# Performance work log

Hardware: AMD Instinct MI355X
Metric: run time of the kernel (lower is better)

## Reference

```python
import jax, jax.numpy as jnp
import numpy as np

E = 768       # embedding_dim
H = 12        # num_heads
ID = 768      # inter_dim
HD = ID // H  # head_dim = 64
DHX = HD // 2  # 32
DHY = HD - DHX  # 32
HP, WP = 16, 16
P = HP * WP
BASE = 10000.0
SCALE = HD ** -0.5


def rot_half(x):
    x1 = x[..., 0::2]
    x2 = x[..., 1::2]
    return jnp.stack([-x2, x1], axis=-1).reshape(x.shape)


def apply_rope(x, cos, sin):
    cos = jnp.repeat(cos, 2, axis=-1)
    sin = jnp.repeat(sin, 2, axis=-1)
    return x * cos + rot_half(x) * sin


def rope_cache(L, dim, base):
    inv_freq = 1.0 / base ** (jnp.arange(0, dim, 2, dtype=jnp.float32) / dim)
    t = jnp.arange(L, dtype=jnp.float32)
    freqs = t[:, None] * inv_freq[None, :]  # [L, dim//2]
    return jnp.cos(freqs), jnp.sin(freqs)


def _rope_tables():
    yy, xx = jnp.meshgrid(jnp.arange(HP), jnp.arange(WP), indexing='ij')
    py = yy.reshape(P)
    px = xx.reshape(P)
    cos_x, sin_x = rope_cache(WP, DHX, BASE)
    cos_y, sin_y = rope_cache(HP, DHY, BASE)
    # gather per-patch tables, shape (1,1,P,1,D/2)
    cx = cos_x[px].reshape(1, 1, P, 1, DHX // 2)
    sx = sin_x[px].reshape(1, 1, P, 1, DHX // 2)
    cy = cos_y[py].reshape(1, 1, P, 1, DHY // 2)
    sy = sin_y[py].reshape(1, 1, P, 1, DHY // 2)
    return cx, sx, cy, sy


def setup_inputs() -> dict:
    key = jax.random.key(0)
    ks = jax.random.split(key, 8)
    B, T = 8, 16
    x = jax.random.normal(ks[0], (B, T, P, E), dtype=jnp.float32)
    s = 0.02
    return {
        'x': x,
        'Wq': jax.random.normal(ks[1], (E, ID), dtype=jnp.float32) * s,
        'bq': jnp.zeros((ID,), dtype=jnp.float32),
        'Wk': jax.random.normal(ks[2], (E, ID), dtype=jnp.float32) * s,
        'bk': jnp.zeros((ID,), dtype=jnp.float32),
        'Wv': jax.random.normal(ks[3], (E, ID), dtype=jnp.float32) * s,
        'bv': jnp.zeros((ID,), dtype=jnp.float32),
        'Wo': jax.random.normal(ks[4], (ID, E), dtype=jnp.float32) * s,
    }


def reference(x, Wq, bq, Wk, bk, Wv, bv, Wo):
    B, T, Pn, _ = x.shape
    q = (x @ Wq + bq).reshape(B, T, Pn, H, HD)
    k = (x @ Wk + bk).reshape(B, T, Pn, H, HD)
    v = (x @ Wv + bv).reshape(B, T, Pn, H, HD)

    cx, sx, cy, sy = _rope_tables()
    qx, qy = q[..., :DHX], q[..., DHX:]
    kx, ky = k[..., :DHX], k[..., DHX:]
    q = jnp.concatenate([apply_rope(qx, cx, sx), apply_rope(qy, cy, sy)], axis=-1)
    k = jnp.concatenate([apply_rope(kx, cx, sx), apply_rope(ky, cy, sy)], axis=-1)

    scores = jnp.einsum('btihd,btjhd->bthij', q, k) * SCALE
    probs = jax.nn.softmax(scores, axis=-1)
    y = jnp.einsum('bthij,btjhd->btihd', probs, v).reshape(B, T, Pn, ID)
    return y @ Wo
```

## Files before the change

kernel.cpp:

```cpp
#include <hip/hip_runtime.h>
#include <hip/hip_bf16.h>
#include <cstdint>
#include <cstddef>

typedef __bf16 bf16;
typedef __bf16 bf16x8 __attribute__((ext_vector_type(8)));
typedef __bf16 bf16x4 __attribute__((ext_vector_type(4)));
typedef float  f32x4  __attribute__((ext_vector_type(4)));

#define MFMA_BF16(a,b,c) __builtin_amdgcn_mfma_f32_16x16x32_bf16((a),(b),(c),0,0,0)

#define BB 8
#define TT 16
#define PP 256
#define EE 768
#define HH 12
#define HDD 64
#define NQKV 2304
#define MROWS 32768

__device__ __forceinline__ void gld_lds16(const bf16* g, bf16* l) {
  __builtin_amdgcn_global_load_lds((const __attribute__((address_space(1))) void*)g,
                                   (__attribute__((address_space(3))) void*)l, 16, 0, 0);
}

__global__ __launch_bounds__(256) void k_cvt_x(const float* __restrict__ x,
                                               bf16* __restrict__ xb) {
  const int64_t i = (int64_t)blockIdx.x * 256 + threadIdx.x;
  const float4* src = (const float4*)x;
  float4 a = src[i * 2];
  float4 b = src[i * 2 + 1];
  bf16x8 o;
  o[0] = (bf16)a.x; o[1] = (bf16)a.y; o[2] = (bf16)a.z; o[3] = (bf16)a.w;
  o[4] = (bf16)b.x; o[5] = (bf16)b.y; o[6] = (bf16)b.z; o[7] = (bf16)b.w;
  *(bf16x8*)(xb + i * 8) = o;
}

__global__ __launch_bounds__(256) void k_wt(const float* __restrict__ Wq,
                                            const float* __restrict__ Wk,
                                            const float* __restrict__ Wv,
                                            const float* __restrict__ Wo,
                                            bf16* __restrict__ wt) {
  __shared__ float tile[32][33];
  const int n0 = blockIdx.x * 32;
  const int k0 = blockIdx.y * 32;
  const float* W;
  int nc;
  if (n0 < 768)        { W = Wq; nc = n0; }
  else if (n0 < 1536)  { W = Wk; nc = n0 - 768; }
  else if (n0 < 2304)  { W = Wv; nc = n0 - 1536; }
  else                 { W = Wo; nc = n0 - 2304; }
  const int tx = threadIdx.x & 31, ty = threadIdx.x >> 5;
  for (int r = ty; r < 32; r += 8)
    tile[r][tx] = W[(int64_t)(k0 + r) * 768 + nc + tx];
  __syncthreads();
  for (int r = ty; r < 32; r += 8)
    wt[(int64_t)(n0 + r) * 768 + k0 + tx] = (bf16)tile[tx][r];
}

__global__ __launch_bounds__(512, 2) void k_qkv(const bf16* __restrict__ xb,
                                                const bf16* __restrict__ wt,
                                                const float* __restrict__ bq,
                                                const float* __restrict__ bk,
                                                const float* __restrict__ bv,
                                                bf16* __restrict__ qb,
                                                bf16* __restrict__ kb,
                                                bf16* __restrict__ vt) {
  extern __shared__ char smem_raw[];
  bf16* smem = (bf16*)smem_raw;
  const int tid = threadIdx.x;
  const int w = tid >> 6, lane = tid & 63, quad = lane >> 4, l16 = lane & 15;
  const int wr = w >> 2, wc = w & 3;
  const int bid = blockIdx.x;
  const int xcd = bid & 7;
  const int loc = bid >> 3;
  const int m0  = (xcd * 16 + loc / 9) * 256;
  const int n0  = (loc % 9) * 256;
  const int cg8 = (((lane & 3) ^ ((lane >> 3) & 3)) * 8);
  const bf16* Ag0 = xb + (int64_t)(m0 + w * 16 + (lane >> 2)) * 768 + cg8;
  const bf16* Bg0 = wt + (int64_t)(n0 + w * 16 + (lane >> 2)) * 768 + cg8;

  auto stage = [&](int kt, int b) {
    bf16* LA = smem + b * 16384 + w * 512;
    bf16* LB = LA + 8192;
    const bf16* GA = Ag0 + kt * 32;
    const bf16* GB = Bg0 + kt * 32;
    gld_lds16(GA, LA);
    gld_lds16(GA + 128 * 768, LA + 4096);
    gld_lds16(GB, LB);
    gld_lds16(GB + 128 * 768, LB + 4096);
  };

  f32x4 acc[8][4] = {};
  stage(0, 0);
  stage(1, 1);
  stage(2, 2);
  const int rkey8 = ((l16 >> 1) & 3) * 8;
  for (int t = 0; t < 24; ++t) {
    if (t < 22)       { asm volatile("s_waitcnt vmcnt(8)" ::: "memory"); }
    else if (t == 22) { asm volatile("s_waitcnt vmcnt(4)" ::: "memory"); }
    else              { asm volatile("s_waitcnt vmcnt(0)" ::: "memory"); }
    __builtin_amdgcn_s_barrier();
    __builtin_amdgcn_sched_barrier(0);
    if (t < 21) stage(t + 3, (t + 3) & 3);
    const bf16* A = smem + (t & 3) * 16384;
    const bf16* B = A + 8192;
    bf16x8 bfr[4];
#pragma unroll
    for (int ni = 0; ni < 4; ++ni)
      bfr[ni] = *(const bf16x8*)&B[(wc * 64 + ni * 16 + l16) * 32 + ((quad * 8) ^ rkey8)];
    bf16x8 afr[8];
#pragma unroll
    for (int mi = 0; mi < 8; ++mi)
      afr[mi] = *(const bf16x8*)&A[(wr * 128 + mi * 16 + l16) * 32 + ((quad * 8) ^ rkey8)];
    __builtin_amdgcn_s_setprio(1);
#pragma unroll
    for (int mi = 0; mi < 8; ++mi)
#pragma unroll
      for (int ni = 0; ni < 4; ++ni)
        acc[mi][ni] = MFMA_BF16(afr[mi], bfr[ni], acc[mi][ni]);
    __builtin_amdgcn_s_setprio(0);
  }
  const int sec = n0 / 768;
  const float* bias_p = (sec == 0) ? bq : (sec == 1) ? bk : bv;
  if (sec == 2) {
#pragma unroll
    for (int ni = 0; ni < 4; ++ni) {
      const int ng = (n0 % 768) + wc * 64 + ni * 16 + l16;
      const int h = ng >> 6, hd = ng & 63;
      const float bias = bias_p[ng];
#pragma unroll
      for (int mi = 0; mi < 8; ++mi) {
        const int rb = m0 + wr * 128 + mi * 16 + quad * 4;
        const int bt = rb >> 8, p = rb & 255;
        bf16x4 pk;
#pragma unroll
        for (int r = 0; r < 4; ++r) pk[r] = (bf16)(acc[mi][ni][r] + bias);
        *(bf16x4*)&vt[((int64_t)(bt * 12 + h) * 64 + hd) * 256 + p] = pk;
      }
    }
  } else {
    bf16* dst = (sec == 0) ? qb : kb;
    const float L2C = 0.83048202372184058696f;
#pragma unroll
    for (int ni = 0; ni < 4; ++ni) {
      const int ng = (n0 % 768) + wc * 64 + ni * 16 + l16;
      const int h = ng >> 6, hd = ng & 63;
      const float bias = bias_p[ng];
      const int j = (hd & 31) >> 1;
      const float invf = exp2f(-(float)j * L2C);
      const bool odd = (hd & 1);
      const bool isx = (hd < 32);
#pragma unroll
      for (int mi = 0; mi < 8; ++mi) {
        const int rb = m0 + wr * 128 + mi * 16 + quad * 4;
        const int bt = rb >> 8;
        const int pb = rb & 255;
#pragma unroll
        for (int r = 0; r < 4; ++r) {
          const int p = pb + r;
          float v = acc[mi][ni][r] + bias;
          float pv = __shfl_xor(v, 1, 64);
          const int pos = isx ? (p & 15) : (p >> 4);
          float sn, cs;
          __sincosf((float)pos * invf, &sn, &cs);
          float o = odd ? (v * cs + pv * sn) : (v * cs - pv * sn);
          dst[((int64_t)(bt * 12 + h) * 256 + p) * 64 + hd] = (bf16)o;
        }
      }
    }
  }
}

__global__ __launch_bounds__(256) void k_attn(bf16* qy,
                                              const bf16* __restrict__ kb,
                                              const bf16* __restrict__ vt) {
  __shared__ __align__(16) bf16 plds[4][16 * 264];
  const int tid = threadIdx.x;
  const int w = tid >> 6, lane = tid & 63, quad = lane >> 4, l16 = lane & 15;
  const int64_t base = (int64_t)blockIdx.x * 16384;
  bf16* Q = qy + base;
  const bf16* K = kb + base;
  const bf16* V = vt + base;
  bf16* pl = plds[w];
  for (int s = 0; s < 4; ++s) {
    const int r0 = w * 64 + s * 16;
    bf16x8 qf0 = *(const bf16x8*)&Q[(r0 + l16) * 64 + quad * 8];
    bf16x8 qf1 = *(const bf16x8*)&Q[(r0 + l16) * 64 + 32 + quad * 8];
    f32x4 sacc[16] = {};
#pragma unroll
    for (int ct = 0; ct < 16; ++ct) {
      bf16x8 kf0 = *(const bf16x8*)&K[(ct * 16 + l16) * 64 + quad * 8];
      bf16x8 kf1 = *(const bf16x8*)&K[(ct * 16 + l16) * 64 + 32 + quad * 8];
      sacc[ct] = MFMA_BF16(qf0, kf0, sacc[ct]);
      sacc[ct] = MFMA_BF16(qf1, kf1, sacc[ct]);
    }
    float mx[4] = {-3e38f, -3e38f, -3e38f, -3e38f};
#pragma unroll
    for (int ct = 0; ct < 16; ++ct)
#pragma unroll
      for (int r = 0; r < 4; ++r) mx[r] = fmaxf(mx[r], sacc[ct][r]);
#pragma unroll
    for (int d = 1; d < 16; d <<= 1)
#pragma unroll
      for (int r = 0; r < 4; ++r) mx[r] = fmaxf(mx[r], __shfl_xor(mx[r], d, 64));
    float sm[4] = {0.f, 0.f, 0.f, 0.f};
#pragma unroll
    for (int ct = 0; ct < 16; ++ct)
#pragma unroll
      for (int r = 0; r < 4; ++r) {
        float e = __expf((sacc[ct][r] - mx[r]) * 0.125f);
        sacc[ct][r] = e;
        sm[r] += e;
      }
#pragma unroll
    for (int d = 1; d < 16; d <<= 1)
#pragma unroll
      for (int r = 0; r < 4; ++r) sm[r] += __shfl_xor(sm[r], d, 64);
#pragma unroll
    for (int ct = 0; ct < 16; ++ct)
#pragma unroll
      for (int r = 0; r < 4; ++r)
        pl[(quad * 4 + r) * 264 + ct * 16 + l16] = (bf16)sacc[ct][r];
    __syncthreads();
    f32x4 oacc[4] = {};
#pragma unroll
    for (int kc = 0; kc < 8; ++kc) {
      bf16x8 pf = *(const bf16x8*)&pl[l16 * 264 + kc * 32 + quad * 8];
#pragma unroll
      for (int nt = 0; nt < 4; ++nt) {
        bf16x8 vf = *(const bf16x8*)&V[(nt * 16 + l16) * 256 + kc * 32 + quad * 8];
        oacc[nt] = MFMA_BF16(pf, vf, oacc[nt]);
      }
    }
    float inv[4];
#pragma unroll
    for (int r = 0; r < 4; ++r) inv[r] = 1.0f / sm[r];
#pragma unroll
    for (int nt = 0; nt < 4; ++nt)
#pragma unroll
      for (int r = 0; r < 4; ++r)
        Q[(r0 + quad * 4 + r) * 64 + nt * 16 + l16] = (bf16)(oacc[nt][r] * inv[r]);
    __syncthreads();
  }
}

__global__ __launch_bounds__(512, 2) void k_out(const bf16* __restrict__ yb,
                                                const bf16* __restrict__ wt,
                                                float* __restrict__ out) {
  extern __shared__ char smem_raw[];
  bf16* smem = (bf16*)smem_raw;
  const int tid = threadIdx.x;
  const int w = tid >> 6, lane = tid & 63, quad = lane >> 4, l16 = lane & 15;
  const int wr = w >> 1, wc = w & 1;
  const int bid = blockIdx.x;
  const int xcd = bid & 7;
  const int loc = bid >> 3;
  const int m0  = (xcd * 16 + loc / 6) * 256;
  const int n0  = (loc % 6) * 128;
  const int bt  = m0 >> 8;
  const int srow = w * 8 + (lane >> 3);
  const int cgo  = (((lane & 7) ^ ((lane >> 3) & 7)) * 8);
  const bf16* Bg0 = wt + (int64_t)(2304 + n0 + srow) * 768 + cgo;

  auto stage = [&](int kt, int p) {
    bf16* LA = smem + p * 24576 + w * 512;
    bf16* LB = smem + p * 24576 + 16384 + w * 512;
    const bf16* GA = yb + (int64_t)(bt * 12 + kt) * 16384 + srow * 64 + cgo;
    const bf16* GB = Bg0 + kt * 64;
#pragma unroll
    for (int rd = 0; rd < 4; ++rd)
      gld_lds16(GA + rd * 4096, LA + rd * 4096);
#pragma unroll
    for (int rd = 0; rd < 2; ++rd)
      gld_lds16(GB + rd * 49152, LB + rd * 4096);
  };

  f32x4 acc[4][4] = {};
  stage(0, 0);
  __syncthreads();
  const int rkey8 = (l16 & 7) * 8;
  for (int t = 0; t < 12; ++t) {
    if (t < 11) stage(t + 1, (t + 1) & 1);
    __builtin_amdgcn_sched_barrier(0);
    const bf16* A = smem + (t & 1) * 24576;
    const bf16* B = A + 16384;
    bf16x8 bfr[4][2];
#pragma unroll
    for (int ni = 0; ni < 4; ++ni)
#pragma unroll
      for (int kk = 0; kk < 2; ++kk)
        bfr[ni][kk] = *(const bf16x8*)&B[(wc * 64 + ni * 16 + l16) * 64 +
                                         (((kk * 4 + quad) * 8) ^ rkey8)];
    bf16x8 afr[4][2];
#pragma unroll
    for (int mi = 0; mi < 4; ++mi)
#pragma unroll
      for (int kk = 0; kk < 2; ++kk)
        afr[mi][kk] = *(const bf16x8*)&A[(wr * 64 + mi * 16 + l16) * 64 +
                                         (((kk * 4 + quad) * 8) ^ rkey8)];
    __builtin_amdgcn_s_setprio(1);
#pragma unroll
    for (int mi = 0; mi < 4; ++mi)
#pragma unroll
      for (int ni = 0; ni < 4; ++ni)
#pragma unroll
        for (int kk = 0; kk < 2; ++kk)
          acc[mi][ni] = MFMA_BF16(afr[mi][kk], bfr[ni][kk], acc[mi][ni]);
    __builtin_amdgcn_s_setprio(0);
    __syncthreads();
  }
#pragma unroll
  for (int mi = 0; mi < 4; ++mi)
#pragma unroll
    for (int ni = 0; ni < 4; ++ni) {
      const int rg = m0 + wr * 64 + mi * 16 + quad * 4;
      const int cg = n0 + wc * 64 + ni * 16 + l16;
#pragma unroll
      for (int r = 0; r < 4; ++r)
        out[(int64_t)(rg + r) * 768 + cg] = acc[mi][ni][r];
    }
}

extern "C" void kernel_launch(void* const* d_in, const int* in_sizes, int n_in,
                              void* d_out, int out_size, void* d_ws, size_t ws_size,
                              hipStream_t stream) {
  const float* x  = (const float*)d_in[0];
  const float* Wq = (const float*)d_in[1];
  const float* bq = (const float*)d_in[2];
  const float* Wk = (const float*)d_in[3];
  const float* bk = (const float*)d_in[4];
  const float* Wv = (const float*)d_in[5];
  const float* bv = (const float*)d_in[6];
  const float* Wo = (const float*)d_in[7];
  float* out = (float*)d_out;

  uint8_t* ws = (uint8_t*)d_ws;
  const size_t SZ = (size_t)25165824 * 2;
  bf16* qy = (bf16*)ws;
  bf16* kb = (bf16*)(ws + SZ);
  bf16* vt = (bf16*)(ws + 2 * SZ);
  bf16* wt = (bf16*)(ws + 3 * SZ);
  bf16* xb = (bf16*)d_out;

  static int attr_set = 0;
  if (!attr_set) {
    (void)hipFuncSetAttribute((const void*)k_qkv,
                              hipFuncAttributeMaxDynamicSharedMemorySize, 131072);
    (void)hipFuncSetAttribute((const void*)k_out,
                              hipFuncAttributeMaxDynamicSharedMemorySize, 98304);
    attr_set = 1;
  }

  k_cvt_x<<<12288, 256, 0, stream>>>(x, xb);
  k_wt<<<dim3(96, 24), 256, 0, stream>>>(Wq, Wk, Wv, Wo, wt);
  k_qkv<<<1152, 512, 131072, stream>>>(xb, wt, bq, bk, bv, qy, kb, vt);
  k_attn<<<1536, 256, 0, stream>>>(qy, kb, vt);
  k_out<<<768, 512, 98304, stream>>>(qy, wt, out);
}
```

Before: 537.0 us.

## Restage QKV GEMM with BK=64 double buffer and LDS-staged coalesced epilogue

```diff
diff --git a/kernel.cpp b/kernel.cpp
--- a/kernel.cpp
+++ b/kernel.cpp
@@ -71,103 +71,146 @@
   const int tid = threadIdx.x;
   const int w = tid >> 6, lane = tid & 63, quad = lane >> 4, l16 = lane & 15;
   const int wr = w >> 2, wc = w & 3;
+  const int kap = l16 & 7;
   const int bid = blockIdx.x;
   const int xcd = bid & 7;
   const int loc = bid >> 3;
   const int m0  = (xcd * 16 + loc / 9) * 256;
   const int n0  = (loc % 9) * 256;
-  const int cg8 = (((lane & 3) ^ ((lane >> 3) & 3)) * 8);
-  const bf16* Ag0 = xb + (int64_t)(m0 + w * 16 + (lane >> 2)) * 768 + cg8;
-  const bf16* Bg0 = wt + (int64_t)(n0 + w * 16 + (lane >> 2)) * 768 + cg8;
-
-  auto stage = [&](int kt, int b) {
-    bf16* LA = smem + b * 16384 + w * 512;
-    bf16* LB = LA + 8192;
-    const bf16* GA = Ag0 + kt * 32;
-    const bf16* GB = Bg0 + kt * 32;
-    gld_lds16(GA, LA);
-    gld_lds16(GA + 128 * 768, LA + 4096);
-    gld_lds16(GB, LB);
-    gld_lds16(GB + 128 * 768, LB + 4096);
+  const int srow = w * 8 + (lane >> 3);
+  const int cgo  = ((lane & 7) ^ ((lane >> 3) & 7)) * 8;
+  const bf16* Ag = xb + (int64_t)(m0 + srow) * 768 + cgo;
+  const bf16* Bg = wt + (int64_t)(n0 + srow) * 768 + cgo;
+
+  auto stage = [&](int kt, int p) {
+    bf16* LA = smem + p * 32768 + w * 512;
+    bf16* LB = LA + 16384;
+    const bf16* GA = Ag + kt * 64;
+    const bf16* GB = Bg + kt * 64;
+#pragma unroll
+    for (int rd = 0; rd < 4; ++rd) {
+      gld_lds16(GA + rd * 49152, LA + rd * 4096);
+      gld_lds16(GB + rd * 49152, LB + rd * 4096);
+    }
   };
 
   f32x4 acc[8][4] = {};
   stage(0, 0);
-  stage(1, 1);
-  stage(2, 2);
-  const int rkey8 = ((l16 >> 1) & 3) * 8;
-  for (int t = 0; t < 24; ++t) {
-    if (t < 22)       { asm volatile("s_waitcnt vmcnt(8)" ::: "memory"); }
-    else if (t == 22) { asm volatile("s_waitcnt vmcnt(4)" ::: "memory"); }
-    else              { asm volatile("s_waitcnt vmcnt(0)" ::: "memory"); }
-    __builtin_amdgcn_s_barrier();
+  __syncthreads();
+  for (int t = 0; t < 12; ++t) {
+    if (t < 11) stage(t + 1, (t + 1) & 1);
     __builtin_amdgcn_sched_barrier(0);
-    if (t < 21) stage(t + 3, (t + 3) & 3);
-    const bf16* A = smem + (t & 3) * 16384;
-    const bf16* B = A + 8192;
-    bf16x8 bfr[4];
+    const bf16* A = smem + (t & 1) * 32768;
+    const bf16* B = A + 16384;
+    bf16x8 bfr[4][2];
 #pragma unroll
     for (int ni = 0; ni < 4; ++ni)
-      bfr[ni] = *(const bf16x8*)&B[(wc * 64 + ni * 16 + l16) * 32 + ((quad * 8) ^ rkey8)];
-    bf16x8 afr[8];
-#pragma unroll
-    for (int mi = 0; mi < 8; ++mi)
-      afr[mi] = *(const bf16x8*)&A[(wr * 128 + mi * 16 + l16) * 32 + ((quad * 8) ^ rkey8)];
-    __builtin_amdgcn_s_setprio(1);
-#pragma unroll
-    for (int mi = 0; mi < 8; ++mi)
-#pragma unroll
-      for (int ni = 0; ni < 4; ++ni)
-        acc[mi][ni] = MFMA_BF16(afr[mi], bfr[ni], acc[mi][ni]);
-    __builtin_amdgcn_s_setprio(0);
+#pragma unroll
+      for (int kk = 0; kk < 2; ++kk)
+        bfr[ni][kk] = *(const bf16x8*)&B[(wc * 64 + ni * 16 + l16) * 64 +
+                                         (((kk * 4 + quad) ^ kap) * 8)];
+#pragma unroll
+    for (int mh = 0; mh < 2; ++mh) {
+      bf16x8 afr[4][2];
+#pragma unroll
+      for (int mi = 0; mi < 4; ++mi)
+#pragma unroll
+        for (int kk = 0; kk < 2; ++kk)
+          afr[mi][kk] = *(const bf16x8*)&A[(wr * 128 + mh * 64 + mi * 16 + l16) * 64 +
+                                           (((kk * 4 + quad) ^ kap) * 8)];
+      __builtin_amdgcn_s_setprio(1);
+#pragma unroll
+      for (int mi = 0; mi < 4; ++mi)
+#pragma unroll
+        for (int ni = 0; ni < 4; ++ni)
+#pragma unroll
+          for (int kk = 0; kk < 2; ++kk)
+            acc[mh * 4 + mi][ni] = MFMA_BF16(afr[mi][kk], bfr[ni][kk], acc[mh * 4 + mi][ni]);
+      __builtin_amdgcn_s_setprio(0);
+    }
+    __syncthreads();
   }
   const int sec = n0 / 768;
+  const int h0 = (n0 % 768) >> 6;
   const float* bias_p = (sec == 0) ? bq : (sec == 1) ? bk : bv;
+  char* eb = (char*)smem;
+  const int64_t obase = (int64_t)(m0 >> 8) * 12 * 16384;
   if (sec == 2) {
 #pragma unroll
     for (int ni = 0; ni < 4; ++ni) {
-      const int ng = (n0 % 768) + wc * 64 + ni * 16 + l16;
-      const int h = ng >> 6, hd = ng & 63;
-      const float bias = bias_p[ng];
+      const int nn = wc * 64 + ni * 16 + l16;
+      const int hh = nn >> 6, hd = nn & 63;
+      const float bias = bias_p[(n0 % 768) + nn];
 #pragma unroll
       for (int mi = 0; mi < 8; ++mi) {
-        const int rb = m0 + wr * 128 + mi * 16 + quad * 4;
-        const int bt = rb >> 8, p = rb & 255;
+        const int p = wr * 128 + mi * 16 + quad * 4;
         bf16x4 pk;
 #pragma unroll
         for (int r = 0; r < 4; ++r) pk[r] = (bf16)(acc[mi][ni][r] + bias);
-        *(bf16x4*)&vt[((int64_t)(bt * 12 + h) * 64 + hd) * 256 + p] = pk;
+        *(bf16x4*)(eb + hh * 32768 + hd * 512 +
+                   ((((p >> 3) ^ (hd & 15)) << 4) | (((p >> 2) & 1) << 3))) = pk;
       }
+    }
+    __syncthreads();
+#pragma unroll
+    for (int it = 0; it < 16; ++it) {
+      const int lin = (it * 512 + tid) * 16;
+      const int hh = lin >> 15;
+      const int rem = lin & 32767;
+      const int hd = rem >> 9;
+      const int cs = (rem >> 4) & 31;
+      const int pc = cs ^ (hd & 15);
+      bf16x8 val = *(const bf16x8*)(eb + lin);
+      *(bf16x8*)&vt[obase + ((int64_t)(h0 + hh) * 64 + hd) * 256 + pc * 8] = val;
     }
   } else {
     bf16* dst = (sec == 0) ? qb : kb;
     const float L2C = 0.83048202372184058696f;
 #pragma unroll
     for (int ni = 0; ni < 4; ++ni) {
-      const int ng = (n0 % 768) + wc * 64 + ni * 16 + l16;
-      const int h = ng >> 6, hd = ng & 63;
-      const float bias = bias_p[ng];
+      const int nn = wc * 64 + ni * 16 + l16;
+      const int hh = nn >> 6, hd = nn & 63;
+      const float bias = bias_p[(n0 % 768) + nn];
       const int j = (hd & 31) >> 1;
       const float invf = exp2f(-(float)j * L2C);
       const bool odd = (hd & 1);
       const bool isx = (hd < 32);
+      float snt[8], cst[8];
+      if (isx) {
+#pragma unroll
+        for (int r = 0; r < 4; ++r)
+          __sincosf((float)(quad * 4 + r) * invf, &snt[r], &cst[r]);
+      } else {
+#pragma unroll
+        for (int mi = 0; mi < 8; ++mi)
+          __sincosf((float)(wr * 8 + mi) * invf, &snt[mi], &cst[mi]);
+      }
 #pragma unroll
       for (int mi = 0; mi < 8; ++mi) {
-        const int rb = m0 + wr * 128 + mi * 16 + quad * 4;
-        const int bt = rb >> 8;
-        const int pb = rb & 255;
 #pragma unroll
         for (int r = 0; r < 4; ++r) {
-          const int p = pb + r;
+          const int p = wr * 128 + mi * 16 + quad * 4 + r;
           float v = acc[mi][ni][r] + bias;
           float pv = __shfl_xor(v, 1, 64);
-          const int pos = isx ? (p & 15) : (p >> 4);
-          float sn, cs;
-          __sincosf((float)pos * invf, &sn, &cs);
-          float o = odd ? (v * cs + pv * sn) : (v * cs - pv * sn);
-          dst[((int64_t)(bt * 12 + h) * 256 + p) * 64 + hd] = (bf16)o;
+          const float sn = isx ? snt[r] : snt[mi];
+          const float cz = isx ? cst[r] : cst[mi];
+          float o = odd ? (v * cz + pv * sn) : (v * cz - pv * sn);
+          *(bf16*)(eb + hh * 32768 + p * 128 +
+                   ((((hd >> 3) ^ (p & 7)) << 4) | ((hd & 7) << 1))) = (bf16)o;
         }
       }
+    }
+    __syncthreads();
+#pragma unroll
+    for (int it = 0; it < 16; ++it) {
+      const int lin = (it * 512 + tid) * 16;
+      const int hh = lin >> 15;
+      const int rem = lin & 32767;
+      const int p = rem >> 7;
+      const int cs = (rem >> 4) & 7;
+      const int hc = cs ^ (p & 7);
+      bf16x8 val = *(const bf16x8*)(eb + lin);
+      *(bf16x8*)&dst[obase + ((int64_t)(h0 + hh) * 256 + p) * 64 + hc * 8] = val;
     }
   }
 }
@@ -188,6 +231,7 @@
     bf16x8 qf0 = *(const bf16x8*)&Q[(r0 + l16) * 64 + quad * 8];
     bf16x8 qf1 = *(const bf16x8*)&Q[(r0 + l16) * 64 + 32 + quad * 8];
     f32x4 sacc[16] = {};
+    __builtin_amdgcn_s_setprio(1);
 #pragma unroll
     for (int ct = 0; ct < 16; ++ct) {
       bf16x8 kf0 = *(const bf16x8*)&K[(ct * 16 + l16) * 64 + quad * 8];
@@ -195,6 +239,7 @@
       sacc[ct] = MFMA_BF16(qf0, kf0, sacc[ct]);
       sacc[ct] = MFMA_BF16(qf1, kf1, sacc[ct]);
     }
+    __builtin_amdgcn_s_setprio(0);
     float mx[4] = {-3e38f, -3e38f, -3e38f, -3e38f};
 #pragma unroll
     for (int ct = 0; ct < 16; ++ct)
@@ -222,8 +267,10 @@
 #pragma unroll
       for (int r = 0; r < 4; ++r)
         pl[(quad * 4 + r) * 264 + ct * 16 + l16] = (bf16)sacc[ct][r];
-    __syncthreads();
+    asm volatile("s_waitcnt lgkmcnt(0)" ::: "memory");
+    __builtin_amdgcn_sched_barrier(0);
     f32x4 oacc[4] = {};
+    __builtin_amdgcn_s_setprio(1);
 #pragma unroll
     for (int kc = 0; kc < 8; ++kc) {
       bf16x8 pf = *(const bf16x8*)&pl[l16 * 264 + kc * 32 + quad * 8];
@@ -233,6 +280,7 @@
         oacc[nt] = MFMA_BF16(pf, vf, oacc[nt]);
       }
     }
+    __builtin_amdgcn_s_setprio(0);
     float inv[4];
 #pragma unroll
     for (int r = 0; r < 4; ++r) inv[r] = 1.0f / sm[r];
@@ -241,7 +289,7 @@
 #pragma unroll
       for (int r = 0; r < 4; ++r)
         Q[(r0 + quad * 4 + r) * 64 + nt * 16 + l16] = (bf16)(oacc[nt][r] * inv[r]);
-    __syncthreads();
+    asm volatile("" ::: "memory");
   }
 }
 
```

Measured after the change: 533.7 us. About the same (-0.6%).
